# Kernel optimization log

Measured on AMD Instinct MI355X. Metric: run time of the kernel, lower is better.

The kernel has to match this reference:

```python
import jax, jax.numpy as jnp
import numpy as np

# static config (mirrors params)
T, B, NA, NF = 48, 256, 23, 4
D = NA * NF          # y_dim = 92
XD = 2               # x_dim
H = 128              # rnn_dim
HD = 128             # h_dim
NL = 2               # n_layers
FS = 0.1
BURN = 12
IN_ENC = XD + D + H  # GRU input size = 222
A0, A1 = 12, 11      # agents 0..11 -> net0, 12..22 -> net1


def setup_inputs() -> dict:
    key = jax.random.key(0)
    ks = jax.random.split(key, 16)
    s = 0.05
    rn = lambda k, shape: jax.random.normal(k, shape, jnp.float32) * s
    return {
        "states": jax.random.normal(ks[0], (T + 1, 1, B, D), jnp.float32),
        # per-network (leading dim 2) GRU layer-0 and layer-1 weights (torch GRU layout: [r|z|n])
        "W_ih0": rn(ks[1], (2, 3 * H, IN_ENC)),
        "W_hh0": rn(ks[2], (2, 3 * H, H)),
        "b_ih0": rn(ks[3], (2, 3 * H)),
        "b_hh0": rn(ks[4], (2, 3 * H)),
        "W_ih1": rn(ks[5], (2, 3 * H, H)),
        "W_hh1": rn(ks[6], (2, 3 * H, H)),
        "b_ih1": rn(ks[7], (2, 3 * H)),
        "b_hh1": rn(ks[8], (2, 3 * H)),
        # decoder MLP (dropout is identity in eval) + mean head
        "W1": rn(ks[9], (2, HD, H)),
        "b1": rn(ks[10], (2, HD)),
        "W2": rn(ks[11], (2, HD, HD)),
        "b2": rn(ks[12], (2, HD)),
        "Wm": rn(ks[13], (2, XD, HD)),
        "bm": rn(ks[14], (2, XD)),
        "rollout": 0,
        "train": 0,
    }


def _gru_cell(x, h, Wih, Whh, bih, bhh):
    gi = x @ Wih.T + bih
    gh = h @ Whh.T + bhh
    r = jax.nn.sigmoid(gi[:, :H] + gh[:, :H])
    z = jax.nn.sigmoid(gi[:, H:2 * H] + gh[:, H:2 * H])
    n = jnp.tanh(gi[:, 2 * H:] + r * gh[:, 2 * H:])
    return (1.0 - z) * n + z * h


def _batch_error(a, b):
    # sum over batch of the euclidean norm over features
    return jnp.sum(jnp.sqrt(jnp.sum((a - b) ** 2, axis=1)))


def _group_step(h, y_t, y3, y3n, lo, hi, g, P):
    # h: [NL, A*B, H]; agents lo..hi-1 of network g, folded into the batch dim
    A = hi - lo
    vel = y3[:, lo:hi, 2:4].transpose(1, 0, 2).reshape(A * B, 2)
    pos = y3[:, lo:hi, 0:2].transpose(1, 0, 2).reshape(A * B, 2)
    vel_true = y3n[:, lo:hi, 2:4].transpose(1, 0, 2).reshape(A * B, 2)
    pos_true = y3n[:, lo:hi, 0:2].transpose(1, 0, 2).reshape(A * B, 2)
    y_rep = jnp.broadcast_to(y_t[None], (A, B, D)).reshape(A * B, D)
    h_last = h[-1]
    enc_in = jnp.concatenate([vel, y_rep, h_last], axis=1)  # [A*B, IN_ENC]
    # decoder uses the PRE-update hidden state
    d = jax.nn.relu(h_last @ P["W1"][g].T + P["b1"][g])
    d = jax.nn.relu(d @ P["W2"][g].T + P["b2"][g])
    dm = d @ P["Wm"][g].T + P["bm"][g]  # [A*B, XD]
    # 2-layer GRU step
    h0n = _gru_cell(enc_in, h[0], P["W_ih0"][g], P["W_hh0"][g], P["b_ih0"][g], P["b_hh0"][g])
    h1n = _gru_cell(h0n, h[1], P["W_ih1"][g], P["W_hh1"][g], P["b_ih1"][g], P["b_hh1"][g])
    h_new = jnp.stack([h0n, h1n])
    L = _batch_error(dm, vel_true)
    ep = _batch_error(pos + vel * FS, pos_true)
    ev = _batch_error(dm[:, :2], vel_true)
    return h_new, L, ep, ev


def _forward(states, P):
    y_seq = states[:T, 0]       # [T, B, D]
    y_next = states[1:T + 1, 0]  # [T, B, D]

    def step(carry, xs):
        h0, h1, L, ep, ev = carry
        y_t, y_t1, t = xs
        y3 = y_t.reshape(B, NA, NF)
        y3n = y_t1.reshape(B, NA, NF)
        h0n, L0, ep0, ev0 = _group_step(h0, y_t, y3, y3n, 0, A0, 0, P)
        h1n, L1, ep1, ev1 = _group_step(h1, y_t, y3, y3n, A0, NA, 1, P)
        m = (t >= BURN).astype(jnp.float32)
        return (h0n, h1n, L + L0 + L1, ep + m * (ep0 + ep1), ev + m * (ev0 + ev1)), None

    init = (jnp.zeros((NL, A0 * B, H), jnp.float32),
            jnp.zeros((NL, A1 * B, H), jnp.float32),
            jnp.zeros((), jnp.float32), jnp.zeros((), jnp.float32), jnp.zeros((), jnp.float32))
    (h0, h1, L, ep, ev), _ = jax.lax.scan(step, init, (y_seq, y_next, jnp.arange(T)))
    L_rec = L / (T * NA)
    e_pos = ep / ((T - BURN) * NA)
    e_vel = ev / ((T - BURN) * NA)
    return L_rec, e_pos, e_vel


def reference(states, W_ih0, W_hh0, b_ih0, b_hh0, W_ih1, W_hh1, b_ih1, b_hh1,
              W1, b1, W2, b2, Wm, bm, rollout, train):
    P = dict(W_ih0=W_ih0, W_hh0=W_hh0, b_ih0=b_ih0, b_hh0=b_hh0,
             W_ih1=W_ih1, W_hh1=W_hh1, b_ih1=b_ih1, b_hh1=b_hh1,
             W1=W1, b1=b1, W2=W2, b2=b2, Wm=Wm, bm=bm)
    return _forward(states, P)
```

## Files before the change

kernel.cpp:

```cpp
#include <hip/hip_runtime.h>
#include <hip/hip_bf16.h>


typedef unsigned short u16;
typedef unsigned int u32;
typedef unsigned char u8;
typedef __attribute__((ext_vector_type(4))) float f32x4;
typedef __attribute__((ext_vector_type(8))) int i32x8;

#define MFMA128(acc, a, b) \
  (acc) = __builtin_amdgcn_mfma_scale_f32_16x16x128_f8f6f4( \
      (a), (b), (acc), 0, 0, 0, 0x7F7F7F7F, 0, 0x7F7F7F7F)

__device__ __forceinline__ i32x8 ld8(const u8* p) { return *(const i32x8*)p; }
__device__ __forceinline__ void pinV(i32x8& x) { asm volatile("" : "+v"(x)); }

__device__ __forceinline__ u8 f2e4(float v) {
  return (u8)(__builtin_amdgcn_cvt_pk_fp8_f32(v, 0.f, 0, false) & 0xff);
}
__device__ __forceinline__ u32 pk4(float a, float b, float c, float d) {
  u32 p = (u32)__builtin_amdgcn_cvt_pk_fp8_f32(a, b, 0, false);
  return (u32)__builtin_amdgcn_cvt_pk_fp8_f32(c, d, (int)p, true);
}
__device__ __forceinline__ float sigf(float x) {
  return __builtin_amdgcn_rcpf(1.f + __expf(-x));
}
__device__ __forceinline__ float tanh_fast(float x) {
  return 1.f - 2.f * __builtin_amdgcn_rcpf(1.f + __expf(2.f * x));
}

__device__ __forceinline__ int swz256(int row, int kq) {
  return (row << 7) + ((kq ^ (row & 3)) << 5);
}
__device__ __forceinline__ int swzU32(int row, int c0) {
  return (row << 7) + ((((c0 >> 5) ^ (row & 3)) << 5) | (c0 & 31));
}

constexpr int E0 = 2 * 384 * 352;
constexpr int E1 = E0 + 2 * 384 * 256;
constexpr int E2 = E1 + 2 * 128 * 128;
constexpr int E3 = E2 + 2 * 128 * 128;
constexpr int E4 = E3 + 2 * 128 * 128;
constexpr int E5 = E4 + 2 * 128 * 128;
constexpr int NBIAS = 2048;
constexpr int TOTAL = E5 + NBIAS + 4;
constexpr int WB_BYTE_OFF = 16384;

constexpr int WB0A_REL = E5;
constexpr int YBG2_REL = WB0A_REL + 23 * 384 * 128;
constexpr int NA1 = TOTAL;
constexpr int NA2 = NA1 + 23 * 384 * 128;
constexpr int NA3 = NA2 + 48 * 256 * 128;

__global__ void prep_kernel(const float* __restrict__ states,
                            const float* __restrict__ Wih0, const float* __restrict__ Whh0,
                            const float* __restrict__ bih0, const float* __restrict__ bhh0,
                            const float* __restrict__ Wih1, const float* __restrict__ Whh1,
                            const float* __restrict__ bih1, const float* __restrict__ bhh1,
                            const float* __restrict__ W1, const float* __restrict__ W2,
                            u8* __restrict__ wb, float* __restrict__ wsf) {
  for (int idx = blockIdx.x * blockDim.x + threadIdx.x; idx < NA3;
       idx += gridDim.x * blockDim.x) {
    if (idx < E0) {
      int g = idx / 135168;
      int r = idx - g * 135168;
      int j = r / 352;
      int k = r - j * 352;
      const float* wi = Wih0 + (g * 384 + j) * 222;
      float v;
      if (k < 94) v = wi[k];
      else if (k < 96) v = 0.f;
      else if (k < 224) v = wi[k - 2];
      else v = Whh0[(g * 384 + j) * 128 + (k - 224)];
      wb[idx] = f2e4(v);
    } else if (idx < E1) {
      int q = idx - E0;
      int g = q / 98304;
      int r = q - g * 98304;
      int j = r >> 8;
      int k = r & 255;
      float v = (k < 128) ? Wih1[(g * 384 + j) * 128 + k]
                          : Whh1[(g * 384 + j) * 128 + (k - 128)];
      wb[idx] = f2e4(v);
    } else if (idx < E2) {
      int q = idx - E1; int g = q >> 14; int r = q & 16383; int j = r >> 7; int k = r & 127;
      wb[idx] = f2e4(W1[(g * 128 + j) * 128 + k]);
    } else if (idx < E3) {
      int q = idx - E2; int g = q >> 14; int r = q & 16383; int j = r >> 7; int k = r & 127;
      wb[idx] = f2e4(W2[(g * 128 + j) * 128 + k]);
    } else if (idx < E5) {
      wb[idx] = 0;
    } else if (idx < E5 + NBIAS) {
      int q = idx - E5;
      float v;
      if (q < 512)       { int g = q >> 8, j = q & 255;              v = bih0[g*384 + j] + bhh0[g*384 + j]; }
      else if (q < 768)  { int p = q - 512;  int g = p >> 7, j = p & 127; v = bih0[g*384 + 256 + j]; }
      else if (q < 1024) { int p = q - 768;  int g = p >> 7, j = p & 127; v = bhh0[g*384 + 256 + j]; }
      else if (q < 1536) { int p = q - 1024; int g = p >> 8, j = p & 255; v = bih1[g*384 + j] + bhh1[g*384 + j]; }
      else if (q < 1792) { int p = q - 1536; int g = p >> 7, j = p & 127; v = bih1[g*384 + 256 + j]; }
      else               { int p = q - 1792; int g = p >> 7, j = p & 127; v = bhh1[g*384 + 256 + j]; }
      wsf[4 + q] = v;
    } else if (idx < TOTAL) {
      wsf[idx - (E5 + NBIAS)] = 0.f;
    } else if (idx < NA2) {
      int q = idx - NA1;
      int a = q / 49152;
      int r = q - a * 49152;
      int j = r >> 7;
      int k = r & 127;
      const float* wi = Wih0 + (((a >= 12) ? 1 : 0) * 384 + j) * 222;
      float v = (k < 92) ? wi[2 + k] : 0.f;
      if (k == a * 4 + 2) v += wi[0];
      if (k == a * 4 + 3) v += wi[1];
      wb[WB0A_REL + q] = f2e4(v);
    } else {
      int q = idx - NA2;
      int t = q >> 15;
      int r = q & 32767;
      int row = r >> 7;
      int k = r & 127;
      float v = (k < 92) ? states[((size_t)t * 256 + row) * 92 + k] : 0.f;
      wb[YBG2_REL + q] = f2e4(v);
    }
  }
}

__global__ __launch_bounds__(512, 2) __attribute__((amdgpu_waves_per_eu(2, 2)))
void rnn_kernel(const float* __restrict__ states,
                const u8* __restrict__ wb,
                float* __restrict__ wsf,
                const float* __restrict__ b1g,
                const float* __restrict__ b2g,
                const float* __restrict__ Wmg,
                const float* __restrict__ bmg) {
  const int blk = blockIdx.x;
  const int g = (blk < 96) ? 0 : 1;
  const int r0 = (g == 0) ? (blk * 32) : ((blk - 96) * 32);
  const int aAg = (g == 0 ? 0 : 12) + (r0 >> 8);
  const int b0 = r0 & 255;

  const int tid = threadIdx.x;
  const int wid = tid >> 6;
  const int ln = tid & 63;
  const int j_in = ln & 15;
  const int kq = ln >> 4;
  const int c0 = wid * 16 + kq * 4;
  const int jh = wid * 16 + j_in;

  __shared__ __align__(64) u8 h0b[2][32 * 128];
  __shared__ __align__(64) u8 h1b[2][32 * 128];
  __shared__ __align__(64) u8 d1b[32 * 128];
  __shared__ __align__(64) u8 d2b[32 * 128];
  __shared__ __align__(16) float bias[1536];
  __shared__ float dmv[48][32][2];
  __shared__ float red[8][3];

  const u8* W0   = wb + g * 135168;
  const u8* W1c  = wb + E0 + g * 98304;
  const u8* Wm1p = wb + E1 + g * 16384;
  const u8* Wm2p = wb + E2 + g * 16384;
  const u8* WB0A = wb + WB0A_REL + aAg * 49152;
  const u8* YBG  = wb + YBG2_REL;

  i32x8 w0r0 = ld8(WB0A + jh * 128 + kq * 32);
  i32x8 w0r1 = ld8(W0 + jh * 352 + 96 + kq * 32);
  i32x8 w0r2 = ld8(W0 + jh * 352 + 224 + kq * 32);
  i32x8 w0z0 = ld8(WB0A + (128 + jh) * 128 + kq * 32);
  i32x8 w0z1 = ld8(W0 + (128 + jh) * 352 + 96 + kq * 32);
  i32x8 w0z2 = ld8(W0 + (128 + jh) * 352 + 224 + kq * 32);
  i32x8 w0n0 = ld8(WB0A + (256 + jh) * 128 + kq * 32);
  i32x8 w0n1 = ld8(W0 + (256 + jh) * 352 + 96 + kq * 32);
  i32x8 wn0  = ld8(W0 + (256 + jh) * 352 + 224 + kq * 32);
  i32x8 w1r0 = ld8(W1c + jh * 256 + kq * 32);
  i32x8 w1r1 = ld8(W1c + jh * 256 + 128 + kq * 32);
  i32x8 w1z0 = ld8(W1c + (128 + jh) * 256 + kq * 32);
  i32x8 w1z1 = ld8(W1c + (128 + jh) * 256 + 128 + kq * 32);
  i32x8 w1n0 = ld8(W1c + (256 + jh) * 256 + kq * 32);
  i32x8 wn1  = ld8(W1c + (256 + jh) * 256 + 128 + kq * 32);
  i32x8 wm1  = ld8(Wm1p + jh * 128 + kq * 32);
  i32x8 wm2  = ld8(Wm2p + jh * 128 + kq * 32);
  pinV(w0r0); pinV(w0r1); pinV(w0r2);
  pinV(w0z0); pinV(w0z1); pinV(w0z2);
  pinV(w0n0); pinV(w0n1); pinV(wn0);
  pinV(w1r0); pinV(w1r1); pinV(w1z0); pinV(w1z1);
  pinV(w1n0); pinV(wn1); pinV(wm1); pinV(wm2);

  for (int i = tid; i < 1536; i += 512) {
    float v;
    if (i < 256)       v = wsf[4 + g * 256 + i];
    else if (i < 384)  v = wsf[516 + g * 128 + (i - 256)];
    else if (i < 512)  v = wsf[772 + g * 128 + (i - 384)];
    else if (i < 768)  v = wsf[1028 + g * 256 + (i - 512)];
    else if (i < 896)  v = wsf[1540 + g * 128 + (i - 768)];
    else if (i < 1024) v = wsf[1796 + g * 128 + (i - 896)];
    else if (i < 1152) v = b1g[g * 128 + (i - 1024)];
    else if (i < 1280) v = b2g[g * 128 + (i - 1152)];
    else               v = Wmg[g * 256 + (i - 1280)];
    bias[i] = v;
  }
  for (int i = tid; i < 32 * 128; i += 512) { h0b[0][i] = 0; h1b[0][i] = 0; }

  f32x4 hv0[2] = {{0,0,0,0},{0,0,0,0}};
  f32x4 hv1[2] = {{0,0,0,0},{0,0,0,0}};
  __syncthreads();

  for (int t = 0; t < 48; ++t) {
    const int cur = t & 1, nxt = cur ^ 1;
    const u8* h0c = h0b[cur]; u8* h0n = h0b[nxt];
    const u8* h1c = h1b[cur]; u8* h1n = h1b[nxt];
    const u8* yt = YBG + t * 32768;

    i32x8 fh1k[2];
    {
      f32x4 b1v = *(const f32x4*)(bias + 1024 + c0);
      f32x4 brv = *(const f32x4*)(bias + c0);
      f32x4 bzv = *(const f32x4*)(bias + 128 + c0);
      f32x4 biv = *(const f32x4*)(bias + 256 + c0);
      f32x4 bhv = *(const f32x4*)(bias + 384 + c0);
#pragma unroll
      for (int nt = 0; nt < 2; ++nt) {
        const int row = nt * 16 + j_in;
        i32x8 fy  = ld8(yt + (b0 + row) * 128 + kq * 32);
        i32x8 fh1 = ld8(h1c + swz256(row, kq));
        i32x8 fh0 = ld8(h0c + swz256(row, kq));
        fh1k[nt] = fh1;
        f32x4 mm = {0,0,0,0};
        MFMA128(mm, wm1, fh1);
        f32x4 aR = {0,0,0,0}, aZ = {0,0,0,0}, aN = {0,0,0,0}, aG = {0,0,0,0};
        MFMA128(aR, w0r0, fy);  MFMA128(aZ, w0z0, fy);  MFMA128(aN, w0n0, fy);
        MFMA128(aR, w0r1, fh1); MFMA128(aZ, w0z1, fh1); MFMA128(aN, w0n1, fh1);
        MFMA128(aR, w0r2, fh0); MFMA128(aZ, w0z2, fh0); MFMA128(aG, wn0, fh0);
        *(u32*)(d1b + swzU32(row, c0)) =
          pk4(fmaxf(mm[0]+b1v[0],0.f), fmaxf(mm[1]+b1v[1],0.f),
              fmaxf(mm[2]+b1v[2],0.f), fmaxf(mm[3]+b1v[3],0.f));
#pragma unroll
        for (int i = 0; i < 4; ++i) {
          float rv = sigf(aR[i] + brv[i]);
          float zv = sigf(aZ[i] + bzv[i]);
          float nv = tanh_fast(aN[i] + biv[i] + rv * (aG[i] + bhv[i]));
          hv0[nt][i] = (1.f - zv) * nv + zv * hv0[nt][i];
        }
        *(u32*)(h0n + swzU32(row, c0)) = pk4(hv0[nt][0], hv0[nt][1], hv0[nt][2], hv0[nt][3]);
      }
    }
    if (t > 0) {
      int row = tid >> 4, c = (tid >> 3) & 1, part = tid & 7;
      const float* wmr = bias + 1280 + c * 128 + part * 16;
      float s = 0.f;
#pragma unroll
      for (int q = 0; q < 4; ++q) {
        u32 w = *(const u32*)(d2b + swzU32(row, part * 16 + q * 4));
        s += wmr[q * 4 + 0] * __builtin_amdgcn_cvt_f32_fp8((int)w, 0);
        s += wmr[q * 4 + 1] * __builtin_amdgcn_cvt_f32_fp8((int)w, 1);
        s += wmr[q * 4 + 2] * __builtin_amdgcn_cvt_f32_fp8((int)w, 2);
        s += wmr[q * 4 + 3] * __builtin_amdgcn_cvt_f32_fp8((int)w, 3);
      }
      s += __shfl_xor(s, 1); s += __shfl_xor(s, 2); s += __shfl_xor(s, 4);
      if (part == 0) dmv[t - 1][row][c] = s;
    }
    __syncthreads();

    {
      f32x4 b2v = *(const f32x4*)(bias + 1152 + c0);
      f32x4 brv = *(const f32x4*)(bias + 512 + c0);
      f32x4 bzv = *(const f32x4*)(bias + 640 + c0);
      f32x4 biv = *(const f32x4*)(bias + 768 + c0);
      f32x4 bhv = *(const f32x4*)(bias + 896 + c0);
#pragma unroll
      for (int nt = 0; nt < 2; ++nt) {
        const int row = nt * 16 + j_in;
        i32x8 fd1 = ld8(d1b + swz256(row, kq));
        i32x8 fg0 = ld8(h0n + swz256(row, kq));
        f32x4 mm = {0,0,0,0};
        MFMA128(mm, wm2, fd1);
        f32x4 aR = {0,0,0,0}, aZ = {0,0,0,0}, aN = {0,0,0,0}, aG = {0,0,0,0};
        MFMA128(aR, w1r0, fg0);      MFMA128(aZ, w1z0, fg0);      MFMA128(aN, w1n0, fg0);
        MFMA128(aR, w1r1, fh1k[nt]); MFMA128(aZ, w1z1, fh1k[nt]); MFMA128(aG, wn1, fh1k[nt]);
        *(u32*)(d2b + swzU32(row, c0)) =
          pk4(fmaxf(mm[0]+b2v[0],0.f), fmaxf(mm[1]+b2v[1],0.f),
              fmaxf(mm[2]+b2v[2],0.f), fmaxf(mm[3]+b2v[3],0.f));
#pragma unroll
        for (int i = 0; i < 4; ++i) {
          float rv = sigf(aR[i] + brv[i]);
          float zv = sigf(aZ[i] + bzv[i]);
          float nv = tanh_fast(aN[i] + biv[i] + rv * (aG[i] + bhv[i]));
          hv1[nt][i] = (1.f - zv) * nv + zv * hv1[nt][i];
        }
        *(u32*)(h1n + swzU32(row, c0)) = pk4(hv1[nt][0], hv1[nt][1], hv1[nt][2], hv1[nt][3]);
      }
    }
    __syncthreads();
  }

  {
    int row = tid >> 4, c = (tid >> 3) & 1, part = tid & 7;
    const float* wmr = bias + 1280 + c * 128 + part * 16;
    float s = 0.f;
#pragma unroll
    for (int q = 0; q < 4; ++q) {
      u32 w = *(const u32*)(d2b + swzU32(row, part * 16 + q * 4));
      s += wmr[q * 4 + 0] * __builtin_amdgcn_cvt_f32_fp8((int)w, 0);
      s += wmr[q * 4 + 1] * __builtin_amdgcn_cvt_f32_fp8((int)w, 1);
      s += wmr[q * 4 + 2] * __builtin_amdgcn_cvt_f32_fp8((int)w, 2);
      s += wmr[q * 4 + 3] * __builtin_amdgcn_cvt_f32_fp8((int)w, 3);
    }
    s += __shfl_xor(s, 1); s += __shfl_xor(s, 2); s += __shfl_xor(s, 4);
    if (part == 0) dmv[47][row][c] = s;
  }
  __syncthreads();

  float accL = 0.f, accEp = 0.f, accEv = 0.f;
  const float bm0 = bmg[g * 2], bm1 = bmg[g * 2 + 1];
  for (int idx = tid; idx < 1536; idx += 512) {
    int t = idx >> 5, row = idx & 31;
    const float* sr = states + ((size_t)(t * 256 + b0 + row)) * 92 + aAg * 4;
    const float* sn = sr + 256 * 92;
    float dx = dmv[t][row][0] + bm0 - sn[2];
    float dy = dmv[t][row][1] + bm1 - sn[3];
    float e = sqrtf(dx * dx + dy * dy);
    accL += e;
    if (t >= 12) {
      accEv += e;
      float ex = sr[0] + 0.1f * sr[2] - sn[0];
      float ey = sr[1] + 0.1f * sr[3] - sn[1];
      accEp += sqrtf(ex * ex + ey * ey);
    }
  }
#pragma unroll
  for (int k = 1; k < 64; k <<= 1) {
    accL  += __shfl_xor(accL, k);
    accEp += __shfl_xor(accEp, k);
    accEv += __shfl_xor(accEv, k);
  }
  if (ln == 0) { red[wid][0] = accL; red[wid][1] = accEp; red[wid][2] = accEv; }
  __syncthreads();
  if (tid < 3) {
    float s = 0.f;
    for (int i = 0; i < 8; ++i) s += red[i][tid];
    atomicAdd(&wsf[tid], s);
  }
}

__global__ void fin_kernel(const float* __restrict__ wacc, float* __restrict__ out) {
  if (threadIdx.x == 0 && blockIdx.x == 0) {
    out[0] = wacc[0] / 1104.f;
    out[1] = wacc[1] / 828.f;
    out[2] = wacc[2] / 828.f;
  }
}

extern "C" void kernel_launch(void* const* d_in, const int* in_sizes, int n_in,
                              void* d_out, int out_size, void* d_ws, size_t ws_size,
                              hipStream_t stream) {
  const float* states = (const float*)d_in[0];
  const float* Wih0 = (const float*)d_in[1];
  const float* Whh0 = (const float*)d_in[2];
  const float* bih0 = (const float*)d_in[3];
  const float* bhh0 = (const float*)d_in[4];
  const float* Wih1 = (const float*)d_in[5];
  const float* Whh1 = (const float*)d_in[6];
  const float* bih1 = (const float*)d_in[7];
  const float* bhh1 = (const float*)d_in[8];
  const float* W1   = (const float*)d_in[9];
  const float* b1   = (const float*)d_in[10];
  const float* W2   = (const float*)d_in[11];
  const float* b2   = (const float*)d_in[12];
  const float* Wm   = (const float*)d_in[13];
  const float* bm   = (const float*)d_in[14];

  float* wsf = (float*)d_ws;
  u8* wb = (u8*)d_ws + WB_BYTE_OFF;

  int prep_blocks = (NA3 + 255) / 256;
  if (prep_blocks > 2048) prep_blocks = 2048;
  prep_kernel<<<prep_blocks, 256, 0, stream>>>(states, Wih0, Whh0, bih0, bhh0,
                                               Wih1, Whh1, bih1, bhh1,
                                               W1, W2, wb, wsf);
  rnn_kernel<<<184, 512, 0, stream>>>(states, wb, wsf, b1, b2, Wm, bm);
  fin_kernel<<<1, 64, 0, stream>>>(wsf, (float*)d_out);
}
```

Before: 278.5 us.

## Prefetch next-step input fragments and refine LDS swizzle to cut bank conflicts

The time loop is unrolled by two through a macro with double-buffered registers. The y_t fragments for step t+1 are now loaded from global memory during the second half of step t, so their latency is hidden behind the layer-1 MFMA work instead of stalling the next step. The LDS swizzle also gains a 16-byte half-swap that depends on bit 2 of the row, and fragments are read as two 16-byte loads, with the aim of removing remaining bank conflicts on the h/d buffers. In exchange it raises register pressure from the extra live fragments and adds address arithmetic.

```diff
diff --git a/kernel.cpp b/kernel.cpp
--- a/kernel.cpp
+++ b/kernel.cpp
@@ -6,6 +6,7 @@
 typedef unsigned int u32;
 typedef unsigned char u8;
 typedef __attribute__((ext_vector_type(4))) float f32x4;
+typedef __attribute__((ext_vector_type(4))) int i32x4;
 typedef __attribute__((ext_vector_type(8))) int i32x8;
 
 #define MFMA128(acc, a, b) \
@@ -29,11 +30,16 @@
   return 1.f - 2.f * __builtin_amdgcn_rcpf(1.f + __expf(2.f * x));
 }
 
-__device__ __forceinline__ int swz256(int row, int kq) {
-  return (row << 7) + ((kq ^ (row & 3)) << 5);
-}
-__device__ __forceinline__ int swzU32(int row, int c0) {
-  return (row << 7) + ((((c0 >> 5) ^ (row & 3)) << 5) | (c0 & 31));
+__device__ __forceinline__ int swzo(int row, int o) {
+  return (row << 7) + ((((o >> 5) ^ row) & 3) << 5) +
+         ((((o >> 4) ^ (row >> 2)) & 1) << 4) + (o & 15);
+}
+__device__ __forceinline__ i32x8 ldfrag(const u8* b, int row, int kq) {
+  const int h = (row >> 2) & 1;
+  const int a = (row << 7) + (((kq ^ row) & 3) << 5);
+  i32x4 lo = *(const i32x4*)(b + a + (h << 4));
+  i32x4 hi = *(const i32x4*)(b + a + ((h ^ 1) << 4));
+  return __builtin_shufflevector(lo, hi, 0, 1, 2, 3, 4, 5, 6, 7);
 }
 
 constexpr int E0 = 2 * 384 * 352;
@@ -204,93 +210,111 @@
   f32x4 hv1[2] = {{0,0,0,0},{0,0,0,0}};
   __syncthreads();
 
-  for (int t = 0; t < 48; ++t) {
-    const int cur = t & 1, nxt = cur ^ 1;
-    const u8* h0c = h0b[cur]; u8* h0n = h0b[nxt];
-    const u8* h1c = h1b[cur]; u8* h1n = h1b[nxt];
-    const u8* yt = YBG + t * 32768;
-
-    i32x8 fh1k[2];
-    {
-      f32x4 b1v = *(const f32x4*)(bias + 1024 + c0);
-      f32x4 brv = *(const f32x4*)(bias + c0);
-      f32x4 bzv = *(const f32x4*)(bias + 128 + c0);
-      f32x4 biv = *(const f32x4*)(bias + 256 + c0);
-      f32x4 bhv = *(const f32x4*)(bias + 384 + c0);
-#pragma unroll
-      for (int nt = 0; nt < 2; ++nt) {
-        const int row = nt * 16 + j_in;
-        i32x8 fy  = ld8(yt + (b0 + row) * 128 + kq * 32);
-        i32x8 fh1 = ld8(h1c + swz256(row, kq));
-        i32x8 fh0 = ld8(h0c + swz256(row, kq));
-        fh1k[nt] = fh1;
-        f32x4 mm = {0,0,0,0};
-        MFMA128(mm, wm1, fh1);
-        f32x4 aR = {0,0,0,0}, aZ = {0,0,0,0}, aN = {0,0,0,0}, aG = {0,0,0,0};
-        MFMA128(aR, w0r0, fy);  MFMA128(aZ, w0z0, fy);  MFMA128(aN, w0n0, fy);
-        MFMA128(aR, w0r1, fh1); MFMA128(aZ, w0z1, fh1); MFMA128(aN, w0n1, fh1);
-        MFMA128(aR, w0r2, fh0); MFMA128(aZ, w0z2, fh0); MFMA128(aG, wn0, fh0);
-        *(u32*)(d1b + swzU32(row, c0)) =
-          pk4(fmaxf(mm[0]+b1v[0],0.f), fmaxf(mm[1]+b1v[1],0.f),
-              fmaxf(mm[2]+b1v[2],0.f), fmaxf(mm[3]+b1v[3],0.f));
-#pragma unroll
-        for (int i = 0; i < 4; ++i) {
-          float rv = sigf(aR[i] + brv[i]);
-          float zv = sigf(aZ[i] + bzv[i]);
-          float nv = tanh_fast(aN[i] + biv[i] + rv * (aG[i] + bhv[i]));
-          hv0[nt][i] = (1.f - zv) * nv + zv * hv0[nt][i];
-        }
-        *(u32*)(h0n + swzU32(row, c0)) = pk4(hv0[nt][0], hv0[nt][1], hv0[nt][2], hv0[nt][3]);
-      }
-    }
-    if (t > 0) {
-      int row = tid >> 4, c = (tid >> 3) & 1, part = tid & 7;
-      const float* wmr = bias + 1280 + c * 128 + part * 16;
-      float s = 0.f;
-#pragma unroll
-      for (int q = 0; q < 4; ++q) {
-        u32 w = *(const u32*)(d2b + swzU32(row, part * 16 + q * 4));
-        s += wmr[q * 4 + 0] * __builtin_amdgcn_cvt_f32_fp8((int)w, 0);
-        s += wmr[q * 4 + 1] * __builtin_amdgcn_cvt_f32_fp8((int)w, 1);
-        s += wmr[q * 4 + 2] * __builtin_amdgcn_cvt_f32_fp8((int)w, 2);
-        s += wmr[q * 4 + 3] * __builtin_amdgcn_cvt_f32_fp8((int)w, 3);
-      }
-      s += __shfl_xor(s, 1); s += __shfl_xor(s, 2); s += __shfl_xor(s, 4);
-      if (part == 0) dmv[t - 1][row][c] = s;
-    }
-    __syncthreads();
-
-    {
-      f32x4 b2v = *(const f32x4*)(bias + 1152 + c0);
-      f32x4 brv = *(const f32x4*)(bias + 512 + c0);
-      f32x4 bzv = *(const f32x4*)(bias + 640 + c0);
-      f32x4 biv = *(const f32x4*)(bias + 768 + c0);
-      f32x4 bhv = *(const f32x4*)(bias + 896 + c0);
-#pragma unroll
-      for (int nt = 0; nt < 2; ++nt) {
-        const int row = nt * 16 + j_in;
-        i32x8 fd1 = ld8(d1b + swz256(row, kq));
-        i32x8 fg0 = ld8(h0n + swz256(row, kq));
-        f32x4 mm = {0,0,0,0};
-        MFMA128(mm, wm2, fd1);
-        f32x4 aR = {0,0,0,0}, aZ = {0,0,0,0}, aN = {0,0,0,0}, aG = {0,0,0,0};
-        MFMA128(aR, w1r0, fg0);      MFMA128(aZ, w1z0, fg0);      MFMA128(aN, w1n0, fg0);
-        MFMA128(aR, w1r1, fh1k[nt]); MFMA128(aZ, w1z1, fh1k[nt]); MFMA128(aG, wn1, fh1k[nt]);
-        *(u32*)(d2b + swzU32(row, c0)) =
-          pk4(fmaxf(mm[0]+b2v[0],0.f), fmaxf(mm[1]+b2v[1],0.f),
-              fmaxf(mm[2]+b2v[2],0.f), fmaxf(mm[3]+b2v[3],0.f));
-#pragma unroll
-        for (int i = 0; i < 4; ++i) {
-          float rv = sigf(aR[i] + brv[i]);
-          float zv = sigf(aZ[i] + bzv[i]);
-          float nv = tanh_fast(aN[i] + biv[i] + rv * (aG[i] + bhv[i]));
-          hv1[nt][i] = (1.f - zv) * nv + zv * hv1[nt][i];
-        }
-        *(u32*)(h1n + swzU32(row, c0)) = pk4(hv1[nt][0], hv1[nt][1], hv1[nt][2], hv1[nt][3]);
-      }
-    }
-    __syncthreads();
-  }
+  i32x8 fyA0 = ld8(YBG + (b0 + j_in) * 128 + kq * 32);
+  i32x8 fyA1 = ld8(YBG + (b0 + 16 + j_in) * 128 + kq * 32);
+  i32x8 fyB0, fyB1;
+
+#define STEP(T, FC0, FC1, FN0, FN1)                                          \
+  {                                                                          \
+    const int cur = (T) & 1, nxt = cur ^ 1;                                  \
+    const u8* h0c = h0b[cur]; u8* h0n = h0b[nxt];                            \
+    const u8* h1c = h1b[cur]; u8* h1n = h1b[nxt];                            \
+    i32x8 fh1k[2];                                                           \
+    {                            \
+      f32x4 b1v = *(const f32x4*)(bias + 1024 + c0);                         \
+      f32x4 brv = *(const f32x4*)(bias + c0);                                \
+      f32x4 bzv = *(const f32x4*)(bias + 128 + c0);                          \
+      f32x4 biv = *(const f32x4*)(bias + 256 + c0);                          \
+      f32x4 bhv = *(const f32x4*)(bias + 384 + c0);                          \
+      _Pragma("unroll")                                                      \
+      for (int nt = 0; nt < 2; ++nt) {                                       \
+        const int row = nt * 16 + j_in;                                      \
+        i32x8 fy  = nt ? (FC1) : (FC0);                                      \
+        i32x8 fh1 = ldfrag(h1c, row, kq);                                    \
+        i32x8 fh0 = ldfrag(h0c, row, kq);                                    \
+        fh1k[nt] = fh1;                                                      \
+        f32x4 mm = {0, 0, 0, 0};                                             \
+        MFMA128(mm, wm1, fh1);                                               \
+        f32x4 aR = {0,0,0,0}, aZ = {0,0,0,0}, aN = {0,0,0,0}, aG = {0,0,0,0};\
+        MFMA128(aR, w0r0, fy);  MFMA128(aZ, w0z0, fy);  MFMA128(aN, w0n0, fy);\
+        MFMA128(aR, w0r1, fh1); MFMA128(aZ, w0z1, fh1); MFMA128(aN, w0n1, fh1);\
+        MFMA128(aR, w0r2, fh0); MFMA128(aZ, w0z2, fh0); MFMA128(aG, wn0, fh0);\
+        *(u32*)(d1b + swzo(row, c0)) =                                       \
+          pk4(fmaxf(mm[0]+b1v[0],0.f), fmaxf(mm[1]+b1v[1],0.f),              \
+              fmaxf(mm[2]+b1v[2],0.f), fmaxf(mm[3]+b1v[3],0.f));             \
+        _Pragma("unroll")                                                    \
+        for (int i = 0; i < 4; ++i) {                                        \
+          float rv = sigf(aR[i] + brv[i]);                                   \
+          float zv = sigf(aZ[i] + bzv[i]);                                   \
+          float nv = tanh_fast(aN[i] + biv[i] + rv * (aG[i] + bhv[i]));      \
+          hv0[nt][i] = (1.f - zv) * nv + zv * hv0[nt][i];                    \
+        }                                                                    \
+        *(u32*)(h0n + swzo(row, c0)) =                                       \
+          pk4(hv0[nt][0], hv0[nt][1], hv0[nt][2], hv0[nt][3]);               \
+      }                                                                      \
+    }                                                                        \
+              \
+    if ((T) > 0) {                                                           \
+      int row = tid >> 4, c = (tid >> 3) & 1, part = tid & 7;                \
+      const float* wmr = bias + 1280 + c * 128 + part * 16;                  \
+      float s = 0.f;                                                         \
+      _Pragma("unroll")                                                      \
+      for (int q = 0; q < 4; ++q) {                                          \
+        u32 w = *(const u32*)(d2b + swzo(row, part * 16 + q * 4));           \
+        s += wmr[q * 4 + 0] * __builtin_amdgcn_cvt_f32_fp8((int)w, 0);       \
+        s += wmr[q * 4 + 1] * __builtin_amdgcn_cvt_f32_fp8((int)w, 1);       \
+        s += wmr[q * 4 + 2] * __builtin_amdgcn_cvt_f32_fp8((int)w, 2);       \
+        s += wmr[q * 4 + 3] * __builtin_amdgcn_cvt_f32_fp8((int)w, 3);       \
+      }                                                                      \
+      s += __shfl_xor(s, 1); s += __shfl_xor(s, 2); s += __shfl_xor(s, 4);   \
+      if (part == 0) dmv[(T) - 1][row][c] = s;                               \
+    }                                                                        \
+    __syncthreads();                                                 \
+    {         \
+      if ((T) < 47) {                                                        \
+        const u8* ytn = YBG + ((T) + 1) * 32768;                             \
+        FN0 = ld8(ytn + (b0 + j_in) * 128 + kq * 32);                        \
+        FN1 = ld8(ytn + (b0 + 16 + j_in) * 128 + kq * 32);                   \
+      }                                                                      \
+      f32x4 b2v = *(const f32x4*)(bias + 1152 + c0);                         \
+      f32x4 brv = *(const f32x4*)(bias + 512 + c0);                          \
+      f32x4 bzv = *(const f32x4*)(bias + 640 + c0);                          \
+      f32x4 biv = *(const f32x4*)(bias + 768 + c0);                          \
+      f32x4 bhv = *(const f32x4*)(bias + 896 + c0);                          \
+      _Pragma("unroll")                                                      \
+      for (int nt = 0; nt < 2; ++nt) {                                       \
+        const int row = nt * 16 + j_in;                                      \
+        i32x8 fd1 = ldfrag(d1b, row, kq);                                    \
+        i32x8 fg0 = ldfrag(h0n, row, kq);                                    \
+        f32x4 mm = {0, 0, 0, 0};                                             \
+        MFMA128(mm, wm2, fd1);                                               \
+        f32x4 aR = {0,0,0,0}, aZ = {0,0,0,0}, aN = {0,0,0,0}, aG = {0,0,0,0};\
+        MFMA128(aR, w1r0, fg0);      MFMA128(aZ, w1z0, fg0);                 \
+        MFMA128(aN, w1n0, fg0);                                              \
+        MFMA128(aR, w1r1, fh1k[nt]); MFMA128(aZ, w1z1, fh1k[nt]);            \
+        MFMA128(aG, wn1, fh1k[nt]);                                          \
+        *(u32*)(d2b + swzo(row, c0)) =                                       \
+          pk4(fmaxf(mm[0]+b2v[0],0.f), fmaxf(mm[1]+b2v[1],0.f),              \
+              fmaxf(mm[2]+b2v[2],0.f), fmaxf(mm[3]+b2v[3],0.f));             \
+        _Pragma("unroll")                                                    \
+        for (int i = 0; i < 4; ++i) {                                        \
+          float rv = sigf(aR[i] + brv[i]);                                   \
+          float zv = sigf(aZ[i] + bzv[i]);                                   \
+          float nv = tanh_fast(aN[i] + biv[i] + rv * (aG[i] + bhv[i]));      \
+          hv1[nt][i] = (1.f - zv) * nv + zv * hv1[nt][i];                    \
+        }                                                                    \
+        *(u32*)(h1n + swzo(row, c0)) =                                       \
+          pk4(hv1[nt][0], hv1[nt][1], hv1[nt][2], hv1[nt][3]);               \
+      }                                                                      \
+    }                                                                        \
+    __syncthreads();                                                 \
+  }
+
+  for (int tq = 0; tq < 24; ++tq) {
+    STEP(tq * 2,     fyA0, fyA1, fyB0, fyB1);
+    STEP(tq * 2 + 1, fyB0, fyB1, fyA0, fyA1);
+  }
+#undef STEP
 
   {
     int row = tid >> 4, c = (tid >> 3) & 1, part = tid & 7;
@@ -298,7 +322,7 @@
     float s = 0.f;
 #pragma unroll
     for (int q = 0; q < 4; ++q) {
-      u32 w = *(const u32*)(d2b + swzU32(row, part * 16 + q * 4));
+      u32 w = *(const u32*)(d2b + swzo(row, part * 16 + q * 4));
       s += wmr[q * 4 + 0] * __builtin_amdgcn_cvt_f32_fp8((int)w, 0);
       s += wmr[q * 4 + 1] * __builtin_amdgcn_cvt_f32_fp8((int)w, 1);
       s += wmr[q * 4 + 2] * __builtin_amdgcn_cvt_f32_fp8((int)w, 2);
```

Measured after the change: 473.0 us. 1.7x slower.
